# Optimization experiments

Measured on AMD Instinct MI355X. Metric: run time of the kernel, lower is better.

## Reference

```python
import jax, jax.numpy as jnp
import numpy as np

N_NODES = 100000
N_EDGES = 500000
IN_DIM, HID, N_CLS = 128, 512, 40


def gcn_conv(x, W, b, src, dst, num_nodes):
    # PyG GCNConv: h = x W; add self-loops; norm = d^-1/2[src] * d^-1/2[dst];
    # out[dst] += norm * h[src]; out += bias
    h = x @ W  # [N, out_dim]
    ones = jnp.ones(src.shape[0], dtype=x.dtype)
    deg = jax.ops.segment_sum(ones, dst, num_segments=num_nodes)  # in-degree incl self-loops
    dinv = jnp.where(deg > 0, jax.lax.rsqrt(deg), 0.0)
    norm = dinv[src] * dinv[dst]  # [E]
    msgs = h[src] * norm[:, None]  # [E, out_dim] gather + scale
    out = jax.ops.segment_sum(msgs, dst, num_segments=num_nodes)
    return out + b


def setup_inputs() -> dict:
    key = jax.random.key(0)
    k1, k2, k3, k4, k5, k6 = jax.random.split(key, 6)
    x = jax.random.normal(k1, (N_NODES, IN_DIM), dtype=jnp.float32)
    edge_index = jax.random.randint(k2, (2, N_EDGES), 0, N_NODES, dtype=jnp.int32)
    # Glorot-ish params
    W1 = jax.random.normal(k3, (IN_DIM, HID), dtype=jnp.float32) * (1.0 / np.sqrt(IN_DIM))
    b1 = jnp.zeros((HID,), dtype=jnp.float32)
    W2 = jax.random.normal(k4, (HID, N_CLS), dtype=jnp.float32) * (1.0 / np.sqrt(HID))
    b2 = jnp.zeros((N_CLS,), dtype=jnp.float32)
    return {"x": x, "edge_index": edge_index, "W1": W1, "b1": b1, "W2": W2, "b2": b2}


def reference(x, edge_index, W1, b1, W2, b2):
    n = x.shape[0]
    # add self-loops once, shared by both conv layers
    loop = jnp.arange(n, dtype=edge_index.dtype)
    src = jnp.concatenate([edge_index[0], loop])
    dst = jnp.concatenate([edge_index[1], loop])
    h = gcn_conv(x, W1, b1, src, dst, n)
    h = jax.nn.relu(h)
    # dropout is identity in eval mode (reference computed in eval)
    h = gcn_conv(h, W2, b2, src, dst, n)
    return jax.nn.log_softmax(h, axis=1)
```

## Files before the change

kernel.cpp:

```cpp
#include <hip/hip_runtime.h>
#include <cstdint>
#include <cstddef>

#define N_NODES 100000
#define N_EDGES 500000
#define IN_DIM  128
#define HID     512
#define N_CLS   40
#define N_SBLK  ((N_NODES + 255) / 256)
#define N_CNTB  ((N_EDGES + 255) / 256)
#define N_XBFB  12500
#define N_PREPB 352

typedef short bf16x8 __attribute__((ext_vector_type(8)));
typedef float f32x4 __attribute__((ext_vector_type(4)));

__device__ inline unsigned short f2bf(float f) {
  unsigned u = __float_as_uint(f);
  u = u + 0x7fffu + ((u >> 16) & 1u);
  return (unsigned short)(u >> 16);
}
__device__ inline float blo(unsigned u) { return __uint_as_float(u << 16); }
__device__ inline float bhi(unsigned u) { return __uint_as_float(u & 0xffff0000u); }

__global__ __launch_bounds__(256) void k_zero(int* __restrict__ cnt, unsigned* __restrict__ flags) {
  int i = blockIdx.x * 256 + threadIdx.x;
  if (i < N_NODES) cnt[i] = 0;
  if (i < 512) flags[i] = 0;
}

__global__ __launch_bounds__(256) void k_count_xbf(const int* __restrict__ dst, int* __restrict__ cnt,
                                                   const float* __restrict__ x, uint2* __restrict__ xb2) {
  int b = blockIdx.x;
  if (b < N_CNTB) {
    int e = b * 256 + threadIdx.x;
    if (e < N_EDGES) atomicAdd(&cnt[dst[e]], 1);
  } else {
    int t = (b - N_CNTB) * 256 + threadIdx.x;
    float4 v = ((const float4*)x)[t];
    uint2 o;
    o.x = (unsigned)f2bf(v.x) | ((unsigned)f2bf(v.y) << 16);
    o.y = (unsigned)f2bf(v.z) | ((unsigned)f2bf(v.w) << 16);
    xb2[t] = o;
  }
}

__global__ __launch_bounds__(256) void k_scan_prep(const int* __restrict__ cnt, unsigned* __restrict__ flags,
                                                   int* __restrict__ offsets, int* __restrict__ cursor,
                                                   float* __restrict__ dinv,
                                                   const float* __restrict__ W1, const float* __restrict__ W2,
                                                   unsigned short* __restrict__ W1F, unsigned short* __restrict__ W2F) {
  int b = blockIdx.x;
  if (b < N_SBLK) {
    __shared__ int s[256];
    __shared__ int base_sh;
    int i = b * 256 + threadIdx.x;
    int v = (i < N_NODES) ? cnt[i] : 0;
    s[threadIdx.x] = v;
    __syncthreads();
    #pragma unroll
    for (int off = 1; off < 256; off <<= 1) {
      int t = (threadIdx.x >= off) ? s[threadIdx.x - off] : 0;
      __syncthreads();
      s[threadIdx.x] += t;
      __syncthreads();
    }
    int incl = s[threadIdx.x];
    if (threadIdx.x == 0)
      base_sh = (int)atomicAdd(&flags[0], (unsigned)s[255]);
    __syncthreads();
    int gbase = base_sh;
    if (i < N_NODES) {
      int excl = gbase + incl - v;
      offsets[i] = excl;
      cursor[i]  = excl;
      dinv[i]    = rsqrtf((float)(v + 1));
    }
  } else {
    int t = (b - N_SBLK) * 256 + threadIdx.x;
    if (t < 65536) {
      int j = t & 7, lane = (t >> 3) & 63, rest = t >> 9;
      int s2 = rest & 3, c = rest >> 2;
      int k = s2 * 32 + (lane >> 4) * 8 + j;
      int n = c * 16 + (lane & 15);
      W1F[t] = f2bf(W1[k * HID + n]);
    } else {
      int u = t - 65536;
      int j = u & 7, lane = (u >> 3) & 63, rest = u >> 9;
      int ct = rest % 3, gk = rest / 3;
      int k = gk * 32 + (lane >> 4) * 8 + j;
      int col = ct * 16 + (lane & 15);
      W2F[u] = (col < N_CLS) ? f2bf(W2[k * N_CLS + col]) : (unsigned short)0;
    }
  }
}

__global__ __launch_bounds__(256) void k_fill(const int* __restrict__ src, const int* __restrict__ dst,
                                              const float* __restrict__ dinv,
                                              int* __restrict__ cursor, int2* __restrict__ epair) {
  int e = blockIdx.x * 256 + threadIdx.x;
  if (e >= N_EDGES) return;
  int s = src[e], d = dst[e];
  int pos = atomicAdd(&cursor[d], 1);
  float nrm = dinv[s] * dinv[d];
  epair[pos] = make_int2(s, __float_as_int(nrm));
}

__global__ __launch_bounds__(256) void k_gather1(const uint2* __restrict__ xb, const int2* __restrict__ ep,
                                                 const int* __restrict__ offsets, const int* __restrict__ cnt,
                                                 const float* __restrict__ dinv, uint2* __restrict__ z1) {
  int lane = threadIdx.x & 63, h = lane >> 5, l = lane & 31;
  int d = blockIdx.x * 8 + (threadIdx.x >> 6) * 2 + h;
  int start = offsets[d], end = start + cnt[d];
  float dd = dinv[d], sl = dd * dd;
  uint2 su = xb[(size_t)d * 32 + l];
  float a0 = sl * blo(su.x), a1 = sl * bhi(su.x), a2 = sl * blo(su.y), a3 = sl * bhi(su.y);
  float p0a = 0.f, p1a = 0.f, p2a = 0.f, p3a = 0.f;
  float q0a = 0.f, q1a = 0.f, q2a = 0.f, q3a = 0.f;
  float r0a = 0.f, r1a = 0.f, r2a = 0.f, r3a = 0.f;

  int i = start;
  for (; i + 3 < end; i += 4) {
    int2 e0 = ep[i], e1 = ep[i + 1], e2 = ep[i + 2], e3 = ep[i + 3];
    uint2 r0 = xb[(size_t)e0.x * 32 + l];
    uint2 r1 = xb[(size_t)e1.x * 32 + l];
    uint2 r2 = xb[(size_t)e2.x * 32 + l];
    uint2 r3 = xb[(size_t)e3.x * 32 + l];
    float n0 = __int_as_float(e0.y), n1 = __int_as_float(e1.y);
    float n2 = __int_as_float(e2.y), n3 = __int_as_float(e3.y);
    a0  += n0 * blo(r0.x); a1  += n0 * bhi(r0.x); a2  += n0 * blo(r0.y); a3  += n0 * bhi(r0.y);
    p0a += n1 * blo(r1.x); p1a += n1 * bhi(r1.x); p2a += n1 * blo(r1.y); p3a += n1 * bhi(r1.y);
    q0a += n2 * blo(r2.x); q1a += n2 * bhi(r2.x); q2a += n2 * blo(r2.y); q3a += n2 * bhi(r2.y);
    r0a += n3 * blo(r3.x); r1a += n3 * bhi(r3.x); r2a += n3 * blo(r3.y); r3a += n3 * bhi(r3.y);
  }
  for (; i < end; ++i) {
    int2 e0 = ep[i];
    uint2 r0 = xb[(size_t)e0.x * 32 + l];
    float n0 = __int_as_float(e0.y);
    a0 += n0 * blo(r0.x); a1 += n0 * bhi(r0.x); a2 += n0 * blo(r0.y); a3 += n0 * bhi(r0.y);
  }
  a0 += p0a + q0a + r0a;
  a1 += p1a + q1a + r1a;
  a2 += p2a + q2a + r2a;
  a3 += p3a + q3a + r3a;
  uint2 o;
  o.x = (unsigned)f2bf(a0) | ((unsigned)f2bf(a1) << 16);
  o.y = (unsigned)f2bf(a2) | ((unsigned)f2bf(a3) << 16);
  z1[(size_t)d * 32 + l] = o;
}

#define HS_STRIDE 56
__global__ __launch_bounds__(64) void k_fused_mfma(const unsigned short* __restrict__ z1b,
                                                   const unsigned short* __restrict__ W1F,
                                                   const float* __restrict__ b1,
                                                   const unsigned short* __restrict__ W2F,
                                                   unsigned short* __restrict__ Pb) {
  __shared__ unsigned short Hs[64 * HS_STRIDE];
  const int lane = threadIdx.x;
  const int c16  = lane & 15, quad = lane >> 4;
  const int odd  = c16 & 1;
  const int mbase = blockIdx.x * 64;

  bf16x8 afrag[4][4];
  #pragma unroll
  for (int t = 0; t < 4; ++t) {
    int mrow = mbase + t * 16 + c16;
    int meff = (mrow < N_NODES) ? mrow : 0;
    const bf16x8* arow = (const bf16x8*)(z1b + (size_t)meff * IN_DIM + quad * 8);
    afrag[t][0] = arow[0];
    afrag[t][1] = arow[4];
    afrag[t][2] = arow[8];
    afrag[t][3] = arow[12];
  }

  f32x4 pacc[4][3];
  #pragma unroll
  for (int t = 0; t < 4; ++t)
    #pragma unroll
    for (int ct = 0; ct < 3; ++ct) pacc[t][ct] = (f32x4){0.f, 0.f, 0.f, 0.f};

  const bf16x8* w1f = (const bf16x8*)W1F;
  const bf16x8* w2f = (const bf16x8*)W2F;
  unsigned short* hs = Hs;

  for (int g = 0; g < 16; ++g) {
    #pragma unroll
    for (int nt = 0; nt < 2; ++nt) {
      int c = g * 2 + nt;
      bf16x8 bp0 = w1f[(c * 4 + 0) * 64 + lane];
      bf16x8 bp1 = w1f[(c * 4 + 1) * 64 + lane];
      bf16x8 bp2 = w1f[(c * 4 + 2) * 64 + lane];
      bf16x8 bp3 = w1f[(c * 4 + 3) * 64 + lane];
      f32x4 h[4];
      #pragma unroll
      for (int t = 0; t < 4; ++t) h[t] = (f32x4){0.f, 0.f, 0.f, 0.f};
      #pragma unroll
      for (int t = 0; t < 4; ++t) h[t] = __builtin_amdgcn_mfma_f32_16x16x32_bf16(afrag[t][0], bp0, h[t], 0, 0, 0);
      #pragma unroll
      for (int t = 0; t < 4; ++t) h[t] = __builtin_amdgcn_mfma_f32_16x16x32_bf16(afrag[t][1], bp1, h[t], 0, 0, 0);
      #pragma unroll
      for (int t = 0; t < 4; ++t) h[t] = __builtin_amdgcn_mfma_f32_16x16x32_bf16(afrag[t][2], bp2, h[t], 0, 0, 0);
      #pragma unroll
      for (int t = 0; t < 4; ++t) h[t] = __builtin_amdgcn_mfma_f32_16x16x32_bf16(afrag[t][3], bp3, h[t], 0, 0, 0);
      float bias = b1[c * 16 + c16];
      int colb = nt * 16 + (c16 & ~1);
      int rb0  = quad * 4 + (odd ? 2 : 0);
      #pragma unroll
      for (int t = 0; t < 4; ++t) {
        float v0 = fmaxf(h[t][0] + bias, 0.f);
        float v1 = fmaxf(h[t][1] + bias, 0.f);
        float v2 = fmaxf(h[t][2] + bias, 0.f);
        float v3 = fmaxf(h[t][3] + bias, 0.f);
        float o0 = __shfl_xor(v0, 1, 64);
        float o1 = __shfl_xor(v1, 1, 64);
        float o2 = __shfl_xor(v2, 1, 64);
        float o3 = __shfl_xor(v3, 1, 64);
        float lo0 = odd ? o2 : v0, hi0 = odd ? v2 : o0;
        float lo1 = odd ? o3 : v1, hi1 = odd ? v3 : o1;
        unsigned p0, p1;
        asm("v_cvt_pk_bf16_f32 %0, %1, %2" : "=v"(p0) : "v"(lo0), "v"(hi0));
        asm("v_cvt_pk_bf16_f32 %0, %1, %2" : "=v"(p1) : "v"(lo1), "v"(hi1));
        *(unsigned*)(hs + (t * 16 + rb0    ) * HS_STRIDE + colb) = p0;
        *(unsigned*)(hs + (t * 16 + rb0 + 1) * HS_STRIDE + colb) = p1;
      }
    }
    bf16x8 hf[4];
    #pragma unroll
    for (int t = 0; t < 4; ++t)
      hf[t] = *(const bf16x8*)(hs + (t * 16 + c16) * HS_STRIDE + quad * 8);
    #pragma unroll
    for (int ct = 0; ct < 3; ++ct) {
      bf16x8 bf = w2f[(g * 3 + ct) * 64 + lane];
      #pragma unroll
      for (int t = 0; t < 4; ++t)
        pacc[t][ct] = __builtin_amdgcn_mfma_f32_16x16x32_bf16(hf[t], bf, pacc[t][ct], 0, 0, 0);
    }
  }

  #pragma unroll
  for (int t = 0; t < 4; ++t) {
    int mrow0 = mbase + t * 16 + quad * 4;
    #pragma unroll
    for (int ct = 0; ct < 3; ++ct) {
      int col = ct * 16 + c16;
      if (col < N_CLS) {
        #pragma unroll
        for (int r = 0; r < 4; ++r) {
          int m = mrow0 + r;
          if (m < N_NODES) Pb[(size_t)m * N_CLS + col] = f2bf(pacc[t][ct][r]);
        }
      }
    }
  }
}

__global__ __launch_bounds__(256) void k_gather2_lsm(const uint2* __restrict__ Pu2,
                                                     const int2* __restrict__ ep,
                                                     const int* __restrict__ offsets, const int* __restrict__ cnt,
                                                     const float* __restrict__ dinv, const float* __restrict__ b2,
                                                     float* __restrict__ out) {
  int lane = threadIdx.x & 63, q = lane >> 4, l = lane & 15;
  int d = blockIdx.x * 16 + (threadIdx.x >> 6) * 4 + q;
  bool act = l < 10;
  int lc = act ? l : 0;
  int start = offsets[d], end = start + cnt[d];
  float dd = dinv[d], sl = dd * dd;

  uint2 su = Pu2[(size_t)d * 10 + lc];
  float a0 = sl * blo(su.x), a1 = sl * bhi(su.x), a2 = sl * blo(su.y), a3 = sl * bhi(su.y);
  float p0a = 0.f, p1a = 0.f, p2a = 0.f, p3a = 0.f;
  float q0a = 0.f, q1a = 0.f, q2a = 0.f, q3a = 0.f;
  float r0a = 0.f, r1a = 0.f, r2a = 0.f, r3a = 0.f;

  int i = start;
  for (; i + 3 < end; i += 4) {
    int2 e0 = ep[i], e1 = ep[i + 1], e2 = ep[i + 2], e3 = ep[i + 3];
    uint2 u0 = Pu2[(size_t)e0.x * 10 + lc];
    uint2 u1 = Pu2[(size_t)e1.x * 10 + lc];
    uint2 u2 = Pu2[(size_t)e2.x * 10 + lc];
    uint2 u3 = Pu2[(size_t)e3.x * 10 + lc];
    float n0 = __int_as_float(e0.y), n1 = __int_as_float(e1.y);
    float n2 = __int_as_float(e2.y), n3 = __int_as_float(e3.y);
    a0  += n0 * blo(u0.x); a1  += n0 * bhi(u0.x); a2  += n0 * blo(u0.y); a3  += n0 * bhi(u0.y);
    p0a += n1 * blo(u1.x); p1a += n1 * bhi(u1.x); p2a += n1 * blo(u1.y); p3a += n1 * bhi(u1.y);
    q0a += n2 * blo(u2.x); q1a += n2 * bhi(u2.x); q2a += n2 * blo(u2.y); q3a += n2 * bhi(u2.y);
    r0a += n3 * blo(u3.x); r1a += n3 * bhi(u3.x); r2a += n3 * blo(u3.y); r3a += n3 * bhi(u3.y);
  }
  for (; i < end; ++i) {
    int2 e0 = ep[i];
    uint2 u0 = Pu2[(size_t)e0.x * 10 + lc];
    float n0 = __int_as_float(e0.y);
    a0 += n0 * blo(u0.x); a1 += n0 * bhi(u0.x); a2 += n0 * blo(u0.y); a3 += n0 * bhi(u0.y);
  }

  float v0, v1, v2, v3;
  if (act) {
    float4 bb = ((const float4*)b2)[l];
    v0 = a0 + p0a + q0a + r0a + bb.x;
    v1 = a1 + p1a + q1a + r1a + bb.y;
    v2 = a2 + p2a + q2a + r2a + bb.z;
    v3 = a3 + p3a + q3a + r3a + bb.w;
  } else {
    v0 = v1 = v2 = v3 = -1e30f;
  }
  float m = fmaxf(fmaxf(v0, v1), fmaxf(v2, v3));
  #pragma unroll
  for (int off = 8; off > 0; off >>= 1) m = fmaxf(m, __shfl_xor(m, off, 64));
  float e = act ? (expf(v0 - m) + expf(v1 - m) + expf(v2 - m) + expf(v3 - m)) : 0.f;
  float s = e;
  #pragma unroll
  for (int off = 8; off > 0; off >>= 1) s += __shfl_xor(s, off, 64);
  float lse = m + logf(s);
  if (act) {
    float4 o = make_float4(v0 - lse, v1 - lse, v2 - lse, v3 - lse);
    ((float4*)(out + (size_t)d * N_CLS))[l] = o;
  }
}

extern "C" void kernel_launch(void* const* d_in, const int* in_sizes, int n_in,
                              void* d_out, int out_size, void* d_ws, size_t ws_size,
                              hipStream_t stream) {
  const float* x  = (const float*)d_in[0];
  const int*   ei = (const int*)d_in[1];
  const int*  src = ei;
  const int*  dst = ei + N_EDGES;
  const float* W1 = (const float*)d_in[2];
  const float* b1 = (const float*)d_in[3];
  const float* W2 = (const float*)d_in[4];
  const float* b2 = (const float*)d_in[5];
  float* out = (float*)d_out;

  float* dinv    = (float*)d_ws;
  int*   cnt     = (int*)(dinv + 131072);
  int*   offsets = cnt + 131072;
  int*   cursor  = offsets + 131072;
  unsigned* flags = (unsigned*)(cursor + 131072);
  int2*  epair   = (int2*)(flags + 1024);
  uint2* xb2     = (uint2*)(epair + 524288);
  unsigned short* Pb = (unsigned short*)xb2;
  unsigned short* z1b = (unsigned short*)(xb2 + 3200000);
  unsigned short* W1F = z1b + (size_t)N_NODES * IN_DIM;
  unsigned short* W2F = W1F + HID * IN_DIM;

  k_zero <<<(N_NODES + 255) / 256, 256, 0, stream>>>(cnt, flags);
  k_count_xbf<<<N_CNTB + N_XBFB, 256, 0, stream>>>(dst, cnt, x, xb2);
  k_scan_prep<<<N_SBLK + N_PREPB, 256, 0, stream>>>(cnt, flags, offsets, cursor, dinv, W1, W2, W1F, W2F);
  k_fill <<<N_CNTB, 256, 0, stream>>>(src, dst, dinv, cursor, epair);
  k_gather1<<<N_NODES / 8, 256, 0, stream>>>(xb2, epair, offsets, cnt, dinv, (uint2*)z1b);
  k_fused_mfma<<<(N_NODES + 63) / 64, 64, 0, stream>>>(z1b, W1F, b1, W2F, Pb);
  k_gather2_lsm<<<N_NODES / 16, 256, 0, stream>>>((const uint2*)Pb, epair, offsets, cnt, dinv, b2, out);
}
```

Baseline: 238.8 us.

## Record per-edge rank during count to drop atomic cursor in CSR fill

The count kernel now saves each edge's atomicAdd return value as its rank within the destination bucket. The fill kernel then computes the slot as offsets[d]+rank[e], which removes the second atomic pass and the cursor array. Independent work is also regrouped across launches: x-to-bf16 conversion moves into the fill kernel and W1/W2 repacking moves into gather1 as extra blocks. The cost is a 500K-int rank array that must be written and read back. Bucket order within each node now matches count order instead of fill order.

After: 226.9 us. 1.05x faster.

```diff
diff --git a/kernel.cpp b/kernel.cpp
--- a/kernel.cpp
+++ b/kernel.cpp
@@ -10,6 +10,7 @@
 #define N_SBLK  ((N_NODES + 255) / 256)
 #define N_CNTB  ((N_EDGES + 255) / 256)
 #define N_XBFB  12500
+#define N_G1B   12500
 #define N_PREPB 352
 
 typedef short bf16x8 __attribute__((ext_vector_type(8)));
@@ -26,15 +27,54 @@
 __global__ __launch_bounds__(256) void k_zero(int* __restrict__ cnt, unsigned* __restrict__ flags) {
   int i = blockIdx.x * 256 + threadIdx.x;
   if (i < N_NODES) cnt[i] = 0;
-  if (i < 512) flags[i] = 0;
-}
-
-__global__ __launch_bounds__(256) void k_count_xbf(const int* __restrict__ dst, int* __restrict__ cnt,
-                                                   const float* __restrict__ x, uint2* __restrict__ xb2) {
+  if (i == 0) flags[0] = 0;
+}
+
+__global__ __launch_bounds__(256) void k_count(const int* __restrict__ dst, int* __restrict__ cnt,
+                                               int* __restrict__ rank) {
+  int e = blockIdx.x * 256 + threadIdx.x;
+  if (e < N_EDGES) rank[e] = atomicAdd(&cnt[dst[e]], 1);
+}
+
+__global__ __launch_bounds__(256) void k_scan(const int* __restrict__ cnt, unsigned* __restrict__ flags,
+                                              int* __restrict__ offsets, float* __restrict__ dinv) {
+  __shared__ int s[256];
+  __shared__ int base_sh;
+  int b = blockIdx.x;
+  int i = b * 256 + threadIdx.x;
+  int v = (i < N_NODES) ? cnt[i] : 0;
+  s[threadIdx.x] = v;
+  __syncthreads();
+  #pragma unroll
+  for (int off = 1; off < 256; off <<= 1) {
+    int t = (threadIdx.x >= off) ? s[threadIdx.x - off] : 0;
+    __syncthreads();
+    s[threadIdx.x] += t;
+    __syncthreads();
+  }
+  int incl = s[threadIdx.x];
+  if (threadIdx.x == 0)
+    base_sh = (int)atomicAdd(&flags[0], (unsigned)s[255]);
+  __syncthreads();
+  if (i < N_NODES) {
+    int excl = base_sh + incl - v;
+    offsets[i] = excl;
+    dinv[i]    = rsqrtf((float)(v + 1));
+  }
+}
+
+__global__ __launch_bounds__(256) void k_fill_xbf(const int* __restrict__ src, const int* __restrict__ dst,
+                                                  const int* __restrict__ rank, const int* __restrict__ offsets,
+                                                  const float* __restrict__ dinv, int2* __restrict__ epair,
+                                                  const float* __restrict__ x, uint2* __restrict__ xb2) {
   int b = blockIdx.x;
   if (b < N_CNTB) {
     int e = b * 256 + threadIdx.x;
-    if (e < N_EDGES) atomicAdd(&cnt[dst[e]], 1);
+    if (e >= N_EDGES) return;
+    int s = src[e], d = dst[e];
+    int pos = offsets[d] + rank[e];
+    float nrm = dinv[s] * dinv[d];
+    epair[pos] = make_int2(s, __float_as_int(nrm));
   } else {
     int t = (b - N_CNTB) * 256 + threadIdx.x;
     float4 v = ((const float4*)x)[t];
@@ -45,39 +85,14 @@
   }
 }
 
-__global__ __launch_bounds__(256) void k_scan_prep(const int* __restrict__ cnt, unsigned* __restrict__ flags,
-                                                   int* __restrict__ offsets, int* __restrict__ cursor,
-                                                   float* __restrict__ dinv,
-                                                   const float* __restrict__ W1, const float* __restrict__ W2,
-                                                   unsigned short* __restrict__ W1F, unsigned short* __restrict__ W2F) {
+__global__ __launch_bounds__(256) void k_gather1(const uint2* __restrict__ xb, const int2* __restrict__ ep,
+                                                 const int* __restrict__ offsets, const int* __restrict__ cnt,
+                                                 const float* __restrict__ dinv, uint2* __restrict__ z1,
+                                                 const float* __restrict__ W1, const float* __restrict__ W2,
+                                                 unsigned short* __restrict__ W1F, unsigned short* __restrict__ W2F) {
   int b = blockIdx.x;
-  if (b < N_SBLK) {
-    __shared__ int s[256];
-    __shared__ int base_sh;
-    int i = b * 256 + threadIdx.x;
-    int v = (i < N_NODES) ? cnt[i] : 0;
-    s[threadIdx.x] = v;
-    __syncthreads();
-    #pragma unroll
-    for (int off = 1; off < 256; off <<= 1) {
-      int t = (threadIdx.x >= off) ? s[threadIdx.x - off] : 0;
-      __syncthreads();
-      s[threadIdx.x] += t;
-      __syncthreads();
-    }
-    int incl = s[threadIdx.x];
-    if (threadIdx.x == 0)
-      base_sh = (int)atomicAdd(&flags[0], (unsigned)s[255]);
-    __syncthreads();
-    int gbase = base_sh;
-    if (i < N_NODES) {
-      int excl = gbase + incl - v;
-      offsets[i] = excl;
-      cursor[i]  = excl;
-      dinv[i]    = rsqrtf((float)(v + 1));
-    }
-  } else {
-    int t = (b - N_SBLK) * 256 + threadIdx.x;
+  if (b >= N_G1B) {
+    int t = (b - N_G1B) * 256 + threadIdx.x;
     if (t < 65536) {
       int j = t & 7, lane = (t >> 3) & 63, rest = t >> 9;
       int s2 = rest & 3, c = rest >> 2;
@@ -92,25 +107,10 @@
       int col = ct * 16 + (lane & 15);
       W2F[u] = (col < N_CLS) ? f2bf(W2[k * N_CLS + col]) : (unsigned short)0;
     }
-  }
-}
-
-__global__ __launch_bounds__(256) void k_fill(const int* __restrict__ src, const int* __restrict__ dst,
-                                              const float* __restrict__ dinv,
-                                              int* __restrict__ cursor, int2* __restrict__ epair) {
-  int e = blockIdx.x * 256 + threadIdx.x;
-  if (e >= N_EDGES) return;
-  int s = src[e], d = dst[e];
-  int pos = atomicAdd(&cursor[d], 1);
-  float nrm = dinv[s] * dinv[d];
-  epair[pos] = make_int2(s, __float_as_int(nrm));
-}
-
-__global__ __launch_bounds__(256) void k_gather1(const uint2* __restrict__ xb, const int2* __restrict__ ep,
-                                                 const int* __restrict__ offsets, const int* __restrict__ cnt,
-                                                 const float* __restrict__ dinv, uint2* __restrict__ z1) {
+    return;
+  }
   int lane = threadIdx.x & 63, h = lane >> 5, l = lane & 31;
-  int d = blockIdx.x * 8 + (threadIdx.x >> 6) * 2 + h;
+  int d = b * 8 + (threadIdx.x >> 6) * 2 + h;
   int start = offsets[d], end = start + cnt[d];
   float dd = dinv[d], sl = dd * dd;
   uint2 su = xb[(size_t)d * 32 + l];
@@ -333,20 +333,21 @@
   float* dinv    = (float*)d_ws;
   int*   cnt     = (int*)(dinv + 131072);
   int*   offsets = cnt + 131072;
-  int*   cursor  = offsets + 131072;
-  unsigned* flags = (unsigned*)(cursor + 131072);
-  int2*  epair   = (int2*)(flags + 1024);
+  unsigned* flags = (unsigned*)(offsets + 131072);
+  int*   rank    = (int*)(flags + 1024);
+  int2*  epair   = (int2*)(rank + 524288);
   uint2* xb2     = (uint2*)(epair + 524288);
   unsigned short* Pb = (unsigned short*)xb2;
   unsigned short* z1b = (unsigned short*)(xb2 + 3200000);
   unsigned short* W1F = z1b + (size_t)N_NODES * IN_DIM;
   unsigned short* W2F = W1F + HID * IN_DIM;
 
-  k_zero <<<(N_NODES + 255) / 256, 256, 0, stream>>>(cnt, flags);
-  k_count_xbf<<<N_CNTB + N_XBFB, 256, 0, stream>>>(dst, cnt, x, xb2);
-  k_scan_prep<<<N_SBLK + N_PREPB, 256, 0, stream>>>(cnt, flags, offsets, cursor, dinv, W1, W2, W1F, W2F);
-  k_fill <<<N_CNTB, 256, 0, stream>>>(src, dst, dinv, cursor, epair);
-  k_gather1<<<N_NODES / 8, 256, 0, stream>>>(xb2, epair, offsets, cnt, dinv, (uint2*)z1b);
+  k_zero    <<<N_SBLK, 256, 0, stream>>>(cnt, flags);
+  k_count   <<<N_CNTB, 256, 0, stream>>>(dst, cnt, rank);
+  k_scan    <<<N_SBLK, 256, 0, stream>>>(cnt, flags, offsets, dinv);
+  k_fill_xbf<<<N_CNTB + N_XBFB, 256, 0, stream>>>(src, dst, rank, offsets, dinv, epair, x, xb2);
+  k_gather1 <<<N_G1B + N_PREPB, 256, 0, stream>>>(xb2, epair, offsets, cnt, dinv, (uint2*)z1b,
+                                                  W1, W2, W1F, W2F);
   k_fused_mfma<<<(N_NODES + 63) / 64, 64, 0, stream>>>(z1b, W1F, b1, W2F, Pb);
   k_gather2_lsm<<<N_NODES / 16, 256, 0, stream>>>((const uint2*)Pb, epair, offsets, cnt, dinv, b2, out);
 }
```
